# Performance work log

Measured on AMD Instinct MI355X. Metric: run time of the kernel, lower is better.

Reference implementation:

```python
import jax, jax.numpy as jnp
import numpy as np
import math
from jax import lax

HIDDEN = 512
BETA = 1.0
MAX_ITERATIONS = 5
CONV_THRESH = 1e-4
SCALE = BETA / math.sqrt(HIDDEN)


def setup_inputs() -> dict:
    key = jax.random.key(0)
    ks = jax.random.split(key, 9)
    B, S, H = 4, 2048, HIDDEN
    w = 1.0 / math.sqrt(H)  # roughly nn.Linear init scale
    return {
        "x": jax.random.normal(ks[0], (B, S, H), jnp.float32),
        "Wq": jax.random.normal(ks[1], (H, H), jnp.float32) * w,
        "bq": jax.random.normal(ks[2], (H,), jnp.float32) * w,
        "Wk": jax.random.normal(ks[3], (H, H), jnp.float32) * w,
        "bk": jax.random.normal(ks[4], (H,), jnp.float32) * w,
        "Wv": jax.random.normal(ks[5], (H, H), jnp.float32) * w,
        "bv": jax.random.normal(ks[6], (H,), jnp.float32) * w,
        "Wo": jax.random.normal(ks[7], (H, H), jnp.float32) * w,
        "bo": jax.random.normal(ks[8], (H,), jnp.float32) * w,
    }


def _hopfield_update(state, keys):
    # scores: [B, S, S]
    scores = jnp.einsum('bsh,bth->bst', state, keys) * SCALE
    attn = jax.nn.softmax(scores, axis=-1)
    return jnp.einsum('bst,bth->bsh', attn, keys)


def reference(x, Wq, bq, Wk, bk, Wv, bv, Wo, bo):
    query = x @ Wq.T + bq
    keys = x @ Wk.T + bk
    values = x @ Wv.T + bv

    # Iterative Hopfield loop: torch breaks after the update that converges.
    # We run a fixed-length scan, freezing state once converged (same math).
    def step(carry, _):
        state, converged, iters = carry
        new_state = _hopfield_update(state, keys)
        # global Frobenius norms, matching torch.norm over the whole tensor
        delta = jnp.linalg.norm(new_state - state) / (jnp.linalg.norm(state) + 1e-8)
        active = jnp.logical_not(converged)
        state = jnp.where(active, new_state, state)
        iters = iters + active.astype(jnp.int32)
        converged = converged | (active & (delta < CONV_THRESH))
        return (state, converged, iters), None

    init = (query, jnp.array(False), jnp.array(0, jnp.int32))
    (state, converged, iterations), _ = lax.scan(step, init, None, length=MAX_ITERATIONS)

    # Final readout attention against values
    scores = jnp.einsum('bsh,bth->bst', state, keys) * SCALE
    attn = jax.nn.softmax(scores, axis=-1)
    out = jnp.einsum('bst,bth->bsh', attn, values)
    out = out @ Wo.T + bo  # dropout p=0.0 / eval: identity
    return out, iterations, converged
```

## Files before the change

### kernel.cpp

```cpp
#include <hip/hip_runtime.h>
#include <hip/hip_bf16.h>
#include <math.h>

#define HH 512
#define BB 4
#define SS 2048
#define NN (BB*SS)
#define SCALE_F 0.04419417382415922f
#define THRESH 1e-4f
#define CTL_FLOATS 1024

typedef __attribute__((ext_vector_type(8))) short bf16x8;
typedef __attribute__((ext_vector_type(4))) float f32x4;

struct Ctl { float sum_d; float sum_o; int iters; int conv; int cur; int bf[10]; };

__device__ __forceinline__ float b2f(unsigned short u) {
    union { unsigned int i; float f; } c; c.i = ((unsigned int)u) << 16; return c.f;
}
__device__ __forceinline__ unsigned short f2b(float f) {
    unsigned int x = __float_as_uint(f);
    unsigned int r = (x + 0x7FFFu + ((x >> 16) & 1u)) >> 16;
    return (unsigned short)r;
}
__device__ __forceinline__ void splitf(float x, unsigned short& h, unsigned short& l) {
    h = f2b(x);
    l = f2b(x - b2f(h));
}
__device__ __forceinline__ f32x4 MF(bf16x8 a, bf16x8 b, f32x4 c) {
    return __builtin_amdgcn_mfma_f32_16x16x32_bf16(a, b, c, 0, 0, 0);
}

#define FBAR() do { \
    asm volatile("s_waitcnt lgkmcnt(0)" ::: "memory"); \
    __builtin_amdgcn_s_barrier(); \
    asm volatile("" ::: "memory"); \
} while (0)

#define LD4(R, ph, pl) do { \
    const unsigned short* _ph = (ph); const unsigned short* _pl = (pl); \
    R##0 = *(const uint4*)(_ph); R##1 = *(const uint4*)(_ph + 8); \
    R##2 = *(const uint4*)(_pl); R##3 = *(const uint4*)(_pl + 8); \
} while (0)
#define ST4(dh, dl, R) do { \
    unsigned short* _dh = (dh); unsigned short* _dl = (dl); \
    *(uint4*)(_dh) = R##0; *(uint4*)(_dh + 8) = R##1; \
    *(uint4*)(_dl) = R##2; *(uint4*)(_dl + 8) = R##3; \
} while (0)

__global__ __launch_bounds__(256) void detect_dtypes(
        const void* p0, const void* p1, const void* p2, const void* p3, const void* p4,
        const void* p5, const void* p6, const void* p7, const void* p8, Ctl* sc)
{
    const void* ps[9] = {p0,p1,p2,p3,p4,p5,p6,p7,p8};
    const int   ns[9] = {NN*HH, HH*HH, HH, HH*HH, HH, HH*HH, HH, HH*HH, HH};
    const int i = blockIdx.x;
    const unsigned short* u = (const unsigned short*)ps[i];
    const int n = ns[i] < 4096 ? ns[i] : 4096;
    __shared__ int cnt;
    if (threadIdx.x == 0) cnt = 0;
    __syncthreads();
    int c = 0;
    for (int j = threadIdx.x; j < n; j += 256) {
        const int e = (u[j] >> 7) & 0xFF;
        if (e < 32 || e >= 224) ++c;
    }
    if (c) atomicAdd(&cnt, c);
    __syncthreads();
    if (threadIdx.x == 0) sc->bf[i] = (cnt * 16 < n) ? 1 : 0;
}

__global__ __launch_bounds__(64) void init_flags(Ctl* sc) {
    if (threadIdx.x == 0) {
        sc->iters = 0; sc->conv = 0; sc->cur = 0; sc->sum_d = 0.f; sc->sum_o = 0.f;
        int any = 0;
        for (int i = 0; i < 9; ++i) any |= sc->bf[i];
        sc->bf[9] = any;
    }
}

__global__ __launch_bounds__(256) void mfma_gemm(
    const void* __restrict__ Xv, int xIdx,
    const void* __restrict__ Wv, int wIdx,
    const void* __restrict__ Bv, int bIdx,
    float* __restrict__ outF, void* __restrict__ outExt,
    unsigned short* __restrict__ pKH, unsigned short* __restrict__ pKL,
    unsigned short* __restrict__ pKTH, unsigned short* __restrict__ pKTL,
    float* __restrict__ S0w, float* __restrict__ S1w,
    int mode, const Ctl* __restrict__ sc)
{
    __shared__ unsigned short Xh[64][72], Xl[64][72], Wh[64][72], Wl[64][72];
    const int tid = threadIdx.x;
    const int cur = sc->cur;
    const void* Xp = (xIdx == -2) ? (const void*)(cur ? S1w : S0w) : Xv;
    const bool xbf = (xIdx >= 0) && (sc->bf[xIdx] != 0);
    const bool wbf = (sc->bf[wIdx] != 0);
    const bool bbf = (sc->bf[bIdx] != 0);
    const bool obf = (mode == 1) && (sc->bf[9] != 0);
    const bool xs = !xbf, ws = !wbf;

    const int m0 = blockIdx.x * 64, n0 = blockIdx.y * 64;
    const int lane = tid & 63, w = tid >> 6;
    const int mi = w & 1, ni = w >> 1;
    const int quad = lane >> 4, l16 = lane & 15;
    const int srow = tid >> 2, skb = (tid & 3) * 16;

    f32x4 acc[2][2];
    #pragma unroll
    for (int a = 0; a < 2; ++a)
        #pragma unroll
        for (int bq = 0; bq < 2; ++bq) acc[a][bq] = (f32x4){0.f, 0.f, 0.f, 0.f};

    for (int kc = 0; kc < HH; kc += 64) {
        __syncthreads();
        {
            float v[16];
            if (xbf) {
                const unsigned short* p = (const unsigned short*)Xp + (size_t)(m0 + srow)*HH + kc + skb;
                #pragma unroll
                for (int i = 0; i < 4; ++i) {
                    ushort4 t = *(const ushort4*)(p + 4*i);
                    v[4*i]=b2f(t.x); v[4*i+1]=b2f(t.y); v[4*i+2]=b2f(t.z); v[4*i+3]=b2f(t.w);
                }
            } else {
                const float* p = (const float*)Xp + (size_t)(m0 + srow)*HH + kc + skb;
                #pragma unroll
                for (int i = 0; i < 4; ++i) {
                    float4 t = *(const float4*)(p + 4*i);
                    v[4*i]=t.x; v[4*i+1]=t.y; v[4*i+2]=t.z; v[4*i+3]=t.w;
                }
            }
            #pragma unroll
            for (int i = 0; i < 4; ++i) {
                unsigned short h[4], l[4];
                #pragma unroll
                for (int j = 0; j < 4; ++j) splitf(v[4*i+j], h[j], l[j]);
                *(ushort4*)&Xh[srow][skb + 4*i] = make_ushort4(h[0], h[1], h[2], h[3]);
                if (xs) *(ushort4*)&Xl[srow][skb + 4*i] = make_ushort4(l[0], l[1], l[2], l[3]);
            }
        }
        {
            float v[16];
            if (wbf) {
                const unsigned short* p = (const unsigned short*)Wv + (size_t)(n0 + srow)*HH + kc + skb;
                #pragma unroll
                for (int i = 0; i < 4; ++i) {
                    ushort4 t = *(const ushort4*)(p + 4*i);
                    v[4*i]=b2f(t.x); v[4*i+1]=b2f(t.y); v[4*i+2]=b2f(t.z); v[4*i+3]=b2f(t.w);
                }
            } else {
                const float* p = (const float*)Wv + (size_t)(n0 + srow)*HH + kc + skb;
                #pragma unroll
                for (int i = 0; i < 4; ++i) {
                    float4 t = *(const float4*)(p + 4*i);
                    v[4*i]=t.x; v[4*i+1]=t.y; v[4*i+2]=t.z; v[4*i+3]=t.w;
                }
            }
            #pragma unroll
            for (int i = 0; i < 4; ++i) {
                unsigned short h[4], l[4];
                #pragma unroll
                for (int j = 0; j < 4; ++j) splitf(v[4*i+j], h[j], l[j]);
                *(ushort4*)&Wh[srow][skb + 4*i] = make_ushort4(h[0], h[1], h[2], h[3]);
                if (ws) *(ushort4*)&Wl[srow][skb + 4*i] = make_ushort4(l[0], l[1], l[2], l[3]);
            }
        }
        __syncthreads();
        #pragma unroll
        for (int d = 0; d < 2; ++d) {
            const int kl = 32*d + quad*8;
            #pragma unroll
            for (int mt = 0; mt < 2; ++mt) {
                const int xr = 32*mi + 16*mt + l16;
                bf16x8 ahx = *(const bf16x8*)&Xh[xr][kl];
                bf16x8 alx;
                if (xs) alx = *(const bf16x8*)&Xl[xr][kl];
                #pragma unroll
                for (int nt = 0; nt < 2; ++nt) {
                    const int wr = 32*ni + 16*nt + l16;
                    bf16x8 bh = *(const bf16x8*)&Wh[wr][kl];
                    acc[mt][nt] = MF(ahx, bh, acc[mt][nt]);
                    if (xs) acc[mt][nt] = MF(alx, bh, acc[mt][nt]);
                    if (ws) {
                        bf16x8 bl = *(const bf16x8*)&Wl[wr][kl];
                        acc[mt][nt] = MF(ahx, bl, acc[mt][nt]);
                    }
                }
            }
        }
    }
    unsigned short* vtH = nullptr;
    if (mode == 4) { vtH = (unsigned short*)(cur ? S0w : S1w); }
    #pragma unroll
    for (int nt = 0; nt < 2; ++nt) {
        const int col = n0 + 32*ni + 16*nt + l16;
        const float bv = bbf ? b2f(((const unsigned short*)Bv)[col]) : ((const float*)Bv)[col];
        #pragma unroll
        for (int mt = 0; mt < 2; ++mt)
            #pragma unroll
            for (int e = 0; e < 4; ++e) {
                const int row = m0 + 32*mi + 16*mt + quad*4 + e;
                const float vv = acc[mt][nt][e] + bv;
                const size_t idx = (size_t)row*HH + col;
                if (mode == 0) outF[idx] = vv;
                else if (mode == 1) {
                    if (obf) ((unsigned short*)outExt)[idx] = f2b(vv);
                    else     ((float*)outExt)[idx] = vv;
                } else {
                    unsigned short h, l; splitf(vv, h, l);
                    const size_t t = ((size_t)(row >> 11) * HH + col) * SS + (row & 2047);
                    if (mode == 3) {
                        pKH[idx] = h; pKL[idx] = l;
                        pKTH[t] = h;  pKTL[t] = l;
                    } else {
                        vtH[t] = h; vtH[(size_t)NN*HH + t] = l;
                    }
                }
            }
    }
}

template<bool FINAL>
__global__ __launch_bounds__(512, 2) void mfma_attn(
    float* __restrict__ S0w, float* __restrict__ S1w,
    const unsigned short* __restrict__ KH, const unsigned short* __restrict__ KL,
    const unsigned short* __restrict__ KTH, const unsigned short* __restrict__ KTL,
    Ctl* sc)
{
    if constexpr (!FINAL) { if (sc->conv) return; }
    const int cur = sc->cur;
    float* Scur = cur ? S1w : S0w;
    float* Out  = FINAL ? Scur : (cur ? S0w : S1w);
    const unsigned short* VTH = FINAL ? (const unsigned short*)(cur ? S0w : S1w) : KTH;
    const unsigned short* VTL = FINAL ? (VTH + (size_t)NN*HH) : KTL;

    __shared__ __align__(16) unsigned short UB0[18432];
    __shared__ __align__(16) unsigned short UB1[18432];
    __shared__ __align__(16) unsigned short SHl[32*520];
    __shared__ __align__(16) unsigned short Pth[32*72], Ptl[32*72];
    __shared__ __align__(16) float Sld[32*68];
    __shared__ __align__(16) float mld[32], lld[32], ald[32];
    __shared__ float redd[8], redo[8];

    const int tid = threadIdx.x;
    const int lane = tid & 63, w = tid >> 6;
    const int quad = lane >> 4, l16 = lane & 15;
    const int r = w & 1, s = w >> 1;

    const int bid = blockIdx.x;
    const int e8 = bid & 7;
    const int b = e8 >> 1;
    const int q0 = 32 * ((bid >> 3) + 32 * (e8 & 1));

    const size_t bSSHH = (size_t)b * SS * HH;
    const size_t bHHSS = (size_t)b * HH * SS;

    const int key = tid >> 3, hs = (tid & 7) * 16;
    const int rw = tid >> 2, k1 = (tid & 3) * 16;

    const unsigned short* pSH = KH + bSSHH + (size_t)key*HH + hs;
    const unsigned short* pSL = KL + bSSHH + (size_t)key*HH + hs;
    const size_t vbase = bHHSS + (size_t)(128*(rw >> 5) + (rw & 31))*SS + k1;
    const unsigned short* pVH = VTH + vbase;
    const unsigned short* pVL = VTL + vbase;

    uint4 Ra0, Ra1, Ra2, Ra3;
    uint4 Rb0, Rb1, Rb2, Rb3;
    LD4(Ra, pSH, pSL);
    LD4(Rb, pSH + 128, pSL + 128);

    bf16x8 ah[16];
    {
        const float* Qr = Scur + ((size_t)b*SS + q0 + 16*r + l16) * HH + quad*8;
        #pragma unroll
        for (int f = 0; f < 16; ++f) {
            float4 v0 = *(const float4*)(Qr + 32*f);
            float4 v1 = *(const float4*)(Qr + 32*f + 4);
            unsigned short h[8], l[8];
            splitf(v0.x,h[0],l[0]); splitf(v0.y,h[1],l[1]); splitf(v0.z,h[2],l[2]); splitf(v0.w,h[3],l[3]);
            splitf(v1.x,h[4],l[4]); splitf(v1.y,h[5],l[5]); splitf(v1.z,h[6],l[6]); splitf(v1.w,h[7],l[7]);
            bf16x8 af;
            #pragma unroll
            for (int j = 0; j < 8; ++j) af[j] = (short)h[j];
            ah[f] = af;
            if (s == 0) {
                unsigned short* d = &SHl[(16*r + l16)*520 + 32*f + quad*8];
                *(ushort4*)(d)     = make_ushort4(l[0], l[1], l[2], l[3]);
                *(ushort4*)(d + 4) = make_ushort4(l[4], l[5], l[6], l[7]);
            }
        }
        if (tid < 32) { mld[tid] = -INFINITY; lld[tid] = 0.f; }
    }

    f32x4 O[8];
    #pragma unroll
    for (int i = 0; i < 8; ++i) O[i] = (f32x4){0.f, 0.f, 0.f, 0.f};

    const int shlbase = (16*r + l16)*520 + quad*8;

    for (int kt = 0; kt < SS/64; ++kt) {
        const size_t so = (size_t)kt*64*HH;
        const size_t po = (size_t)kt*64;
        f32x4 sA = (f32x4){0.f,0.f,0.f,0.f}, sB = (f32x4){0.f,0.f,0.f,0.f};
        #pragma unroll
        for (int c = 0; c < 4; ++c) {
            unsigned short* ub = (c & 1) ? UB1 : UB0;
            if ((c & 1) == 0) {
                ST4(ub + key*136 + hs, ub + 8704 + key*136 + hs, Ra);
                if (c == 0) LD4(Ra, pSH + so + 2*128, pSL + so + 2*128);
                else        LD4(Ra, pVH + po, pVL + po);
            } else {
                ST4(ub + key*136 + hs, ub + 8704 + key*136 + hs, Rb);
                if (c == 1) LD4(Rb, pSH + so + 3*128, pSL + so + 3*128);
                else        LD4(Rb, pVH + (size_t)32*SS + po, pVL + (size_t)32*SS + po);
            }
            FBAR();
            #pragma unroll
            for (int kf = 0; kf < 4; ++kf) {
                bf16x8 alf = *(const bf16x8*)&SHl[shlbase + c*128 + kf*32];
                const int c0 = kf*32 + quad*8;
                bf16x8 bh = *(const bf16x8*)&ub[(16*s + l16)*136 + c0];
                bf16x8 bl = *(const bf16x8*)&ub[8704 + (16*s + l16)*136 + c0];
                const bf16x8 a = ah[c*4 + kf];
                if (kf & 1) {
                    sB = MF(a, bh, sB); sB = MF(alf, bh, sB); sB = MF(a, bl, sB);
                } else {
                    sA = MF(a, bh, sA); sA = MF(alf, bh, sA); sA = MF(a, bl, sA);
                }
            }
        }
        f32x4 sacc = sA + sB;
        #pragma unroll
        for (int e = 0; e < 4; ++e)
            Sld[(16*r + quad*4 + e)*68 + 16*s + l16] = sacc[e] * SCALE_F;
        FBAR();
        {
            const int row = tid >> 4, sg = tid & 15;
            const float* sr = Sld + row*68 + sg*4;
            float4 x0 = *(const float4*)(sr);
            float mt = fmaxf(fmaxf(x0.x, x0.y), fmaxf(x0.z, x0.w));
            #pragma unroll
            for (int mk = 1; mk < 16; mk <<= 1) mt = fmaxf(mt, __shfl_xor(mt, mk, 16));
            const float mprev = mld[row];
            const float mnew = fmaxf(mprev, mt);
            float p[4];
            p[0]=__expf(x0.x-mnew); p[1]=__expf(x0.y-mnew); p[2]=__expf(x0.z-mnew); p[3]=__expf(x0.w-mnew);
            float ps = p[0]+p[1]+p[2]+p[3];
            #pragma unroll
            for (int mk = 1; mk < 16; mk <<= 1) ps += __shfl_xor(ps, mk, 16);
            const float alpha = __expf(mprev - mnew);
            if (sg == 0) { mld[row] = mnew; lld[row] = lld[row]*alpha + ps; ald[row] = alpha; }
            unsigned short h[4], l[4];
            #pragma unroll
            for (int i = 0; i < 4; ++i) splitf(p[i], h[i], l[i]);
            *(ushort4*)&Pth[row*72 + sg*4] = make_ushort4(h[0],h[1],h[2],h[3]);
            *(ushort4*)&Ptl[row*72 + sg*4] = make_ushort4(l[0],l[1],l[2],l[3]);
        }
        FBAR();
        {
            const float4 av = *(const float4*)&ald[16*r + 4*quad];
            const float a4[4] = {av.x, av.y, av.z, av.w};
            #pragma unroll
            for (int i = 0; i < 8; ++i)
                #pragma unroll
                for (int e = 0; e < 4; ++e) O[i][e] *= a4[e];
        }
        bf16x8 pah[2], pal[2];
        #pragma unroll
        for (int kf = 0; kf < 2; ++kf) {
            pah[kf] = *(const bf16x8*)&Pth[(16*r + l16)*72 + kf*32 + quad*8];
            pal[kf] = *(const bf16x8*)&Ptl[(16*r + l16)*72 + kf*32 + quad*8];
        }
        #pragma unroll
        for (int c = 0; c < 4; ++c) {
            unsigned short* ub = (c & 1) ? UB1 : UB0;
            if ((c & 1) == 0) {
                ST4(ub + rw*72 + k1, ub + 9216 + rw*72 + k1, Ra);
                if (c == 0)             LD4(Ra, pVH + (size_t)64*SS + po, pVL + (size_t)64*SS + po);
                else if (kt+1 < SS/64)  LD4(Ra, pSH + so + (size_t)64*HH,
                                             pSL + so + (size_t)64*HH);
            } else {
                ST4(ub + rw*72 + k1, ub + 9216 + rw*72 + k1, Rb);
                if (c == 1)             LD4(Rb, pVH + (size_t)96*SS + po, pVL + (size_t)96*SS + po);
                else if (kt+1 < SS/64)  LD4(Rb, pSH + so + (size_t)64*HH + 128,
                                             pSL + so + (size_t)64*HH + 128);
            }
            FBAR();
            #pragma unroll
            for (int nt = 0; nt < 2; ++nt) {
                const int rb = (32*s + 16*nt + l16)*72;
                #pragma unroll
                for (int kf = 0; kf < 2; ++kf) {
                    bf16x8 bh = *(const bf16x8*)&ub[rb + kf*32 + quad*8];
                    bf16x8 bl = *(const bf16x8*)&ub[9216 + rb + kf*32 + quad*8];
                    O[c*2+nt] = MF(pah[kf], bh, O[c*2+nt]);
                    O[c*2+nt] = MF(pal[kf], bh, O[c*2+nt]);
                    O[c*2+nt] = MF(pah[kf], bl, O[c*2+nt]);
                }
            }
        }
    }
    const float4 lv = *(const float4*)&lld[16*r + 4*quad];
    const float inv[4] = {1.f/lv.x, 1.f/lv.y, 1.f/lv.z, 1.f/lv.w};
    float pd = 0.f, po2 = 0.f;
    #pragma unroll
    for (int c = 0; c < 4; ++c)
        #pragma unroll
        for (int nt = 0; nt < 2; ++nt)
            #pragma unroll
            for (int e = 0; e < 4; ++e) {
                const int row = q0 + 16*r + quad*4 + e;
                const int col = 128*s + 32*c + 16*nt + l16;
                const float nv = O[c*2+nt][e] * inv[e];
                const size_t idx = (size_t)b*SS*HH + (size_t)row*HH + col;
                if constexpr (!FINAL) {
                    const float old = Scur[idx];
                    const float d = nv - old;
                    pd += d*d; po2 += old*old;
                }
                Out[idx] = nv;
            }
    if constexpr (!FINAL) {
        #pragma unroll
        for (int mk = 1; mk < 64; mk <<= 1) {
            pd  += __shfl_xor(pd, mk, 64);
            po2 += __shfl_xor(po2, mk, 64);
        }
        if (lane == 0) { redd[w] = pd; redo[w] = po2; }
        __syncthreads();
        if (tid == 0) {
            float td = 0.f, to = 0.f;
            #pragma unroll
            for (int i = 0; i < 8; ++i) { td += redd[i]; to += redo[i]; }
            atomicAdd(&sc->sum_d, td);
            atomicAdd(&sc->sum_o, to);
        }
    }
}

__global__ __launch_bounds__(64) void flag_update(Ctl* sc) {
    if (threadIdx.x != 0) return;
    if (sc->conv) return;
    sc->cur ^= 1;
    sc->iters += 1;
    const float delta = sqrtf(sc->sum_d) / (sqrtf(sc->sum_o) + 1e-8f);
    if (delta < THRESH) sc->conv = 1;
    sc->sum_d = 0.f; sc->sum_o = 0.f;
}

__global__ __launch_bounds__(64) void write_scalars(const Ctl* sc, void* outv) {
    if (threadIdx.x != 0) return;
    if (sc->bf[9]) {
        unsigned short* o = (unsigned short*)outv;
        o[(size_t)NN*HH]     = f2b((float)sc->iters);
        o[(size_t)NN*HH + 1] = f2b(sc->conv ? 1.0f : 0.0f);
    } else {
        float* o = (float*)outv;
        o[(size_t)NN*HH]     = (float)sc->iters;
        o[(size_t)NN*HH + 1] = sc->conv ? 1.0f : 0.0f;
    }
}

extern "C" void kernel_launch(void* const* d_in, const int* in_sizes, int n_in,
                              void* d_out, int out_size, void* d_ws, size_t ws_size,
                              hipStream_t stream)
{
    const void* x  = d_in[0];
    const void* Wq = d_in[1];
    const void* bq = d_in[2];
    const void* Wk = d_in[3];
    const void* bk = d_in[4];
    const void* Wv = d_in[5];
    const void* bv = d_in[6];
    const void* Wo = d_in[7];
    const void* bo = d_in[8];

    Ctl* sc = (Ctl*)d_ws;
    float* S0 = (float*)d_ws + CTL_FLOATS;
    float* S1 = S0 + (size_t)NN*HH;
    unsigned short* KH  = (unsigned short*)(S1 + (size_t)NN*HH);
    unsigned short* KL  = KH  + (size_t)NN*HH;
    unsigned short* KTH = KL  + (size_t)NN*HH;
    unsigned short* KTL = KTH + (size_t)NN*HH;

    const dim3 ggrid(NN/64, HH/64);
    const int  agrid = 256;

    detect_dtypes<<<9, 256, 0, stream>>>(x, Wq, bq, Wk, bk, Wv, bv, Wo, bo, sc);
    init_flags<<<1, 64, 0, stream>>>(sc);

    mfma_gemm<<<ggrid, 256, 0, stream>>>(x, 0, Wq, 1, bq, 2, S0, nullptr,
                                         nullptr, nullptr, nullptr, nullptr, S0, S1, 0, sc);
    mfma_gemm<<<ggrid, 256, 0, stream>>>(x, 0, Wk, 3, bk, 4, nullptr, nullptr,
                                         KH, KL, KTH, KTL, S0, S1, 3, sc);

    for (int it = 0; it < 5; ++it) {
        mfma_attn<false><<<agrid, 512, 0, stream>>>(S0, S1, KH, KL, KTH, KTL, sc);
        flag_update<<<1, 64, 0, stream>>>(sc);
    }

    mfma_gemm<<<ggrid, 256, 0, stream>>>(x, 0, Wv, 5, bv, 6, nullptr, nullptr,
                                         nullptr, nullptr, nullptr, nullptr, S0, S1, 4, sc);
    mfma_attn<true><<<agrid, 512, 0, stream>>>(S0, S1, KH, KL, KTH, KTL, sc);
    mfma_gemm<<<ggrid, 256, 0, stream>>>(nullptr, -2, Wo, 7, bo, 8, nullptr, d_out,
                                         nullptr, nullptr, nullptr, nullptr, S0, S1, 1, sc);
    if (out_size >= (int)((size_t)NN*HH + 2))
        write_scalars<<<1, 64, 0, stream>>>(sc, d_out);
}
```

Measured before the change: 1.277 ms.

## Stage K/V tiles in two larger chunks and keep query low parts in registers

The attention kernel now stages each 64-key tile in two half-width chunks of 256 hidden columns instead of four 128-column chunks. This halves the barriers per phase, and each thread loads twice as many bytes per prefetch. The low-precision query split is held in registers (al[16]) instead of shared memory, which removes an LDS read per MFMA group. The cost is much higher register pressure (eight uint4 staging registers plus sixteen more bf16x8) and larger LDS buffers, which may reduce occupancy under launch_bounds(512,2) or cause spills.

```diff
diff --git a/kernel.cpp b/kernel.cpp
--- a/kernel.cpp
+++ b/kernel.cpp
@@ -37,15 +37,19 @@
     asm volatile("" ::: "memory"); \
 } while (0)
 
-#define LD4(R, ph, pl) do { \
+#define LD8(R, ph, pl) do { \
     const unsigned short* _ph = (ph); const unsigned short* _pl = (pl); \
-    R##0 = *(const uint4*)(_ph); R##1 = *(const uint4*)(_ph + 8); \
-    R##2 = *(const uint4*)(_pl); R##3 = *(const uint4*)(_pl + 8); \
+    R##0 = *(const uint4*)(_ph);      R##1 = *(const uint4*)(_ph + 8); \
+    R##2 = *(const uint4*)(_ph + 16); R##3 = *(const uint4*)(_ph + 24); \
+    R##4 = *(const uint4*)(_pl);      R##5 = *(const uint4*)(_pl + 8); \
+    R##6 = *(const uint4*)(_pl + 16); R##7 = *(const uint4*)(_pl + 24); \
 } while (0)
-#define ST4(dh, dl, R) do { \
+#define ST8(dh, dl, R) do { \
     unsigned short* _dh = (dh); unsigned short* _dl = (dl); \
-    *(uint4*)(_dh) = R##0; *(uint4*)(_dh + 8) = R##1; \
-    *(uint4*)(_dl) = R##2; *(uint4*)(_dl + 8) = R##3; \
+    *(uint4*)(_dh)      = R##0; *(uint4*)(_dh + 8)  = R##1; \
+    *(uint4*)(_dh + 16) = R##2; *(uint4*)(_dh + 24) = R##3; \
+    *(uint4*)(_dl)      = R##4; *(uint4*)(_dl + 8)  = R##5; \
+    *(uint4*)(_dl + 16) = R##6; *(uint4*)(_dl + 24) = R##7; \
 } while (0)
 
 __global__ __launch_bounds__(256) void detect_dtypes(
@@ -234,9 +238,8 @@
     const unsigned short* VTH = FINAL ? (const unsigned short*)(cur ? S0w : S1w) : KTH;
     const unsigned short* VTL = FINAL ? (VTH + (size_t)NN*HH) : KTL;
 
-    __shared__ __align__(16) unsigned short UB0[18432];
-    __shared__ __align__(16) unsigned short UB1[18432];
-    __shared__ __align__(16) unsigned short SHl[32*520];
+    __shared__ __align__(16) unsigned short UB0[34816];
+    __shared__ __align__(16) unsigned short UB1[34816];
     __shared__ __align__(16) unsigned short Pth[32*72], Ptl[32*72];
     __shared__ __align__(16) float Sld[32*68];
     __shared__ __align__(16) float mld[32], lld[32], ald[32];
@@ -255,21 +258,19 @@
     const size_t bSSHH = (size_t)b * SS * HH;
     const size_t bHHSS = (size_t)b * HH * SS;
 
-    const int key = tid >> 3, hs = (tid & 7) * 16;
-    const int rw = tid >> 2, k1 = (tid & 3) * 16;
+    const int key = tid >> 3, hs = (tid & 7) * 32;
+    const int rw2 = tid >> 1, kc2 = (tid & 1) * 32;
 
     const unsigned short* pSH = KH + bSSHH + (size_t)key*HH + hs;
     const unsigned short* pSL = KL + bSSHH + (size_t)key*HH + hs;
-    const size_t vbase = bHHSS + (size_t)(128*(rw >> 5) + (rw & 31))*SS + k1;
-    const unsigned short* pVH = VTH + vbase;
-    const unsigned short* pVL = VTL + vbase;
-
-    uint4 Ra0, Ra1, Ra2, Ra3;
-    uint4 Rb0, Rb1, Rb2, Rb3;
-    LD4(Ra, pSH, pSL);
-    LD4(Rb, pSH + 128, pSL + 128);
-
-    bf16x8 ah[16];
+    const int vhid0 = 128*(rw2 >> 6) + 32*((rw2 >> 5) & 1) + (rw2 & 31);
+    const unsigned short* pVH = VTH + bHHSS + (size_t)vhid0*SS + kc2;
+    const unsigned short* pVL = VTL + bHHSS + (size_t)vhid0*SS + kc2;
+
+    uint4 Ra0, Ra1, Ra2, Ra3, Ra4, Ra5, Ra6, Ra7;
+    LD8(Ra, pSH, pSL);
+
+    bf16x8 ah[16], al[16];
     {
         const float* Qr = Scur + ((size_t)b*SS + q0 + 16*r + l16) * HH + quad*8;
         #pragma unroll
@@ -279,15 +280,10 @@
             unsigned short h[8], l[8];
             splitf(v0.x,h[0],l[0]); splitf(v0.y,h[1],l[1]); splitf(v0.z,h[2],l[2]); splitf(v0.w,h[3],l[3]);
             splitf(v1.x,h[4],l[4]); splitf(v1.y,h[5],l[5]); splitf(v1.z,h[6],l[6]); splitf(v1.w,h[7],l[7]);
-            bf16x8 af;
-            #pragma unroll
-            for (int j = 0; j < 8; ++j) af[j] = (short)h[j];
-            ah[f] = af;
-            if (s == 0) {
-                unsigned short* d = &SHl[(16*r + l16)*520 + 32*f + quad*8];
-                *(ushort4*)(d)     = make_ushort4(l[0], l[1], l[2], l[3]);
-                *(ushort4*)(d + 4) = make_ushort4(l[4], l[5], l[6], l[7]);
-            }
+            bf16x8 af, bf;
+            #pragma unroll
+            for (int j = 0; j < 8; ++j) { af[j] = (short)h[j]; bf[j] = (short)l[j]; }
+            ah[f] = af; al[f] = bf;
         }
         if (tid < 32) { mld[tid] = -INFINITY; lld[tid] = 0.f; }
     }
@@ -295,37 +291,29 @@
     f32x4 O[8];
     #pragma unroll
     for (int i = 0; i < 8; ++i) O[i] = (f32x4){0.f, 0.f, 0.f, 0.f};
-
-    const int shlbase = (16*r + l16)*520 + quad*8;
 
     for (int kt = 0; kt < SS/64; ++kt) {
         const size_t so = (size_t)kt*64*HH;
         const size_t po = (size_t)kt*64;
         f32x4 sA = (f32x4){0.f,0.f,0.f,0.f}, sB = (f32x4){0.f,0.f,0.f,0.f};
         #pragma unroll
-        for (int c = 0; c < 4; ++c) {
-            unsigned short* ub = (c & 1) ? UB1 : UB0;
-            if ((c & 1) == 0) {
-                ST4(ub + key*136 + hs, ub + 8704 + key*136 + hs, Ra);
-                if (c == 0) LD4(Ra, pSH + so + 2*128, pSL + so + 2*128);
-                else        LD4(Ra, pVH + po, pVL + po);
-            } else {
-                ST4(ub + key*136 + hs, ub + 8704 + key*136 + hs, Rb);
-                if (c == 1) LD4(Rb, pSH + so + 3*128, pSL + so + 3*128);
-                else        LD4(Rb, pVH + (size_t)32*SS + po, pVL + (size_t)32*SS + po);
-            }
+        for (int p = 0; p < 2; ++p) {
+            unsigned short* ub = p ? UB1 : UB0;
+            ST8(ub + key*260 + hs, ub + 16640 + key*260 + hs, Ra);
+            if (p == 0) LD8(Ra, pSH + so + 256, pSL + so + 256);
+            else        LD8(Ra, pVH + po, pVL + po);
             FBAR();
             #pragma unroll
-            for (int kf = 0; kf < 4; ++kf) {
-                bf16x8 alf = *(const bf16x8*)&SHl[shlbase + c*128 + kf*32];
+            for (int kf = 0; kf < 8; ++kf) {
                 const int c0 = kf*32 + quad*8;
-                bf16x8 bh = *(const bf16x8*)&ub[(16*s + l16)*136 + c0];
-                bf16x8 bl = *(const bf16x8*)&ub[8704 + (16*s + l16)*136 + c0];
-                const bf16x8 a = ah[c*4 + kf];
+                bf16x8 bh = *(const bf16x8*)&ub[(16*s + l16)*260 + c0];
+                bf16x8 bl = *(const bf16x8*)&ub[16640 + (16*s + l16)*260 + c0];
+                const bf16x8 a  = ah[8*p + kf];
+                const bf16x8 af = al[8*p + kf];
                 if (kf & 1) {
-                    sB = MF(a, bh, sB); sB = MF(alf, bh, sB); sB = MF(a, bl, sB);
+                    sB = MF(a, bh, sB); sB = MF(af, bh, sB); sB = MF(a, bl, sB);
                 } else {
-                    sA = MF(a, bh, sA); sA = MF(alf, bh, sA); sA = MF(a, bl, sA);
+                    sA = MF(a, bh, sA); sA = MF(af, bh, sA); sA = MF(a, bl, sA);
                 }
             }
         }
@@ -372,32 +360,27 @@
             pal[kf] = *(const bf16x8*)&Ptl[(16*r + l16)*72 + kf*32 + quad*8];
         }
         #pragma unroll
-        for (int c = 0; c < 4; ++c) {
-            unsigned short* ub = (c & 1) ? UB1 : UB0;
-            if ((c & 1) == 0) {
-                ST4(ub + rw*72 + k1, ub + 9216 + rw*72 + k1, Ra);
-                if (c == 0)             LD4(Ra, pVH + (size_t)64*SS + po, pVL + (size_t)64*SS + po);
-                else if (kt+1 < SS/64)  LD4(Ra, pSH + so + (size_t)64*HH,
-                                             pSL + so + (size_t)64*HH);
-            } else {
-                ST4(ub + rw*72 + k1, ub + 9216 + rw*72 + k1, Rb);
-                if (c == 1)             LD4(Rb, pVH + (size_t)96*SS + po, pVL + (size_t)96*SS + po);
-                else if (kt+1 < SS/64)  LD4(Rb, pSH + so + (size_t)64*HH + 128,
-                                             pSL + so + (size_t)64*HH + 128);
-            }
+        for (int p = 0; p < 2; ++p) {
+            unsigned short* ub = p ? UB1 : UB0;
+            ST8(ub + rw2*68 + kc2, ub + 17408 + rw2*68 + kc2, Ra);
+            if (p == 0)             LD8(Ra, pVH + (size_t)64*SS + po, pVL + (size_t)64*SS + po);
+            else if (kt+1 < SS/64)  LD8(Ra, pSH + so + (size_t)64*HH, pSL + so + (size_t)64*HH);
             FBAR();
             #pragma unroll
-            for (int nt = 0; nt < 2; ++nt) {
-                const int rb = (32*s + 16*nt + l16)*72;
-                #pragma unroll
-                for (int kf = 0; kf < 2; ++kf) {
-                    bf16x8 bh = *(const bf16x8*)&ub[rb + kf*32 + quad*8];
-                    bf16x8 bl = *(const bf16x8*)&ub[9216 + rb + kf*32 + quad*8];
-                    O[c*2+nt] = MF(pah[kf], bh, O[c*2+nt]);
-                    O[c*2+nt] = MF(pal[kf], bh, O[c*2+nt]);
-                    O[c*2+nt] = MF(pah[kf], bl, O[c*2+nt]);
-                }
-            }
+            for (int cp = 0; cp < 2; ++cp)
+                #pragma unroll
+                for (int nt = 0; nt < 2; ++nt) {
+                    const int rb = (64*s + 32*cp + 16*nt + l16)*68;
+                    const int oi = (2*p + cp)*2 + nt;
+                    #pragma unroll
+                    for (int kf = 0; kf < 2; ++kf) {
+                        bf16x8 bh = *(const bf16x8*)&ub[rb + kf*32 + quad*8];
+                        bf16x8 bl = *(const bf16x8*)&ub[17408 + rb + kf*32 + quad*8];
+                        O[oi] = MF(pah[kf], bh, O[oi]);
+                        O[oi] = MF(pal[kf], bh, O[oi]);
+                        O[oi] = MF(pah[kf], bl, O[oi]);
+                    }
+                }
         }
     }
     const float4 lv = *(const float4*)&lld[16*r + 4*quad];
```

New measurement: 4.407 ms. 3.45x slower.

## Stage K/V tiles via direct global-to-LDS loads with XOR swizzle

Applied to the files above, without the earlier changes.

Replaces the register-staged global loads plus LDS stores in the attention kernel with global_load_lds direct-to-LDS transfers, double-buffered across UB0/UB1. Padded LDS layouts are replaced by unpadded tiles with an XOR swizzle to avoid bank conflicts, which shrinks the shared buffers. This removes VGPR pressure and explicit ds_write instructions, at the cost of waiting on vmcnt(0) at every barrier, so prefetch depth is limited to one stage.

```diff
diff --git a/kernel.cpp b/kernel.cpp
--- a/kernel.cpp
+++ b/kernel.cpp
@@ -31,21 +31,21 @@
     return __builtin_amdgcn_mfma_f32_16x16x32_bf16(a, b, c, 0, 0, 0);
 }
 
+typedef __attribute__((address_space(1))) const unsigned int gu32;
+typedef __attribute__((address_space(3))) unsigned int lu32;
+__device__ __forceinline__ void gl_lds16(const unsigned short* g, unsigned short* l) {
+    __builtin_amdgcn_global_load_lds((gu32*)g, (lu32*)l, 16, 0, 0);
+}
+
+#define SBAR() do { \
+    asm volatile("s_waitcnt vmcnt(0) lgkmcnt(0)" ::: "memory"); \
+    __builtin_amdgcn_s_barrier(); \
+    asm volatile("" ::: "memory"); \
+} while (0)
 #define FBAR() do { \
     asm volatile("s_waitcnt lgkmcnt(0)" ::: "memory"); \
     __builtin_amdgcn_s_barrier(); \
     asm volatile("" ::: "memory"); \
-} while (0)
-
-#define LD4(R, ph, pl) do { \
-    const unsigned short* _ph = (ph); const unsigned short* _pl = (pl); \
-    R##0 = *(const uint4*)(_ph); R##1 = *(const uint4*)(_ph + 8); \
-    R##2 = *(const uint4*)(_pl); R##3 = *(const uint4*)(_pl + 8); \
-} while (0)
-#define ST4(dh, dl, R) do { \
-    unsigned short* _dh = (dh); unsigned short* _dl = (dl); \
-    *(uint4*)(_dh) = R##0; *(uint4*)(_dh + 8) = R##1; \
-    *(uint4*)(_dl) = R##2; *(uint4*)(_dl + 8) = R##3; \
 } while (0)
 
 __global__ __launch_bounds__(256) void detect_dtypes(
@@ -234,8 +234,8 @@
     const unsigned short* VTH = FINAL ? (const unsigned short*)(cur ? S0w : S1w) : KTH;
     const unsigned short* VTL = FINAL ? (VTH + (size_t)NN*HH) : KTL;
 
-    __shared__ __align__(16) unsigned short UB0[18432];
-    __shared__ __align__(16) unsigned short UB1[18432];
+    __shared__ __align__(16) unsigned short UB0[16384];
+    __shared__ __align__(16) unsigned short UB1[16384];
     __shared__ __align__(16) unsigned short SHl[32*520];
     __shared__ __align__(16) unsigned short Pth[32*72], Ptl[32*72];
     __shared__ __align__(16) float Sld[32*68];
@@ -255,19 +255,32 @@
     const size_t bSSHH = (size_t)b * SS * HH;
     const size_t bHHSS = (size_t)b * HH * SS;
 
-    const int key = tid >> 3, hs = (tid & 7) * 16;
-    const int rw = tid >> 2, k1 = (tid & 3) * 16;
-
-    const unsigned short* pSH = KH + bSSHH + (size_t)key*HH + hs;
-    const unsigned short* pSL = KL + bSSHH + (size_t)key*HH + hs;
-    const size_t vbase = bHHSS + (size_t)(128*(rw >> 5) + (rw & 31))*SS + k1;
-    const unsigned short* pVH = VTH + vbase;
-    const unsigned short* pVL = VTL + vbase;
-
-    uint4 Ra0, Ra1, Ra2, Ra3;
-    uint4 Rb0, Rb1, Rb2, Rb3;
-    LD4(Ra, pSH, pSL);
-    LD4(Rb, pSH + 128, pSL + 128);
+    const int keyS = 4*w + quad;
+    const int swS  = ((lane & 15) ^ (keyS & 7)) * 8;
+    const int r3   = lane >> 3;
+    const int swP  = ((lane & 7) ^ (r3 & 7)) * 8;
+    const int rowP = 8*w + r3;
+    const int hidP0 = 128*(rowP >> 5) + (rowP & 31);
+    const int hidP1 = 128*(2 + (rowP >> 5)) + (rowP & 31);
+
+    auto stageS = [&](int c, int kt, unsigned short* ub) {
+        const size_t g0 = bSSHH + (size_t)(kt*64 + keyS)*HH + c*128 + swS;
+        const size_t g1 = bSSHH + (size_t)(kt*64 + keyS + 32)*HH + c*128 + swS;
+        gl_lds16(KH + g0, ub +                 w*64*8);
+        gl_lds16(KH + g1, ub +        4096 +   w*64*8);
+        gl_lds16(KL + g0, ub + 8192 +          w*64*8);
+        gl_lds16(KL + g1, ub + 8192 + 4096 +   w*64*8);
+    };
+    auto stageP = [&](int c, int kt, unsigned short* ub) {
+        const size_t g0 = bHHSS + (size_t)(hidP0 + 32*c)*SS + (size_t)kt*64 + swP;
+        const size_t g1 = bHHSS + (size_t)(hidP1 + 32*c)*SS + (size_t)kt*64 + swP;
+        gl_lds16(VTH + g0, ub +                 w*64*8);
+        gl_lds16(VTH + g1, ub +        4096 +   w*64*8);
+        gl_lds16(VTL + g0, ub + 8192 +          w*64*8);
+        gl_lds16(VTL + g1, ub + 8192 + 4096 +   w*64*8);
+    };
+
+    stageS(0, 0, UB0);
 
     bf16x8 ah[16];
     {
@@ -299,28 +312,19 @@
     const int shlbase = (16*r + l16)*520 + quad*8;
 
     for (int kt = 0; kt < SS/64; ++kt) {
-        const size_t so = (size_t)kt*64*HH;
-        const size_t po = (size_t)kt*64;
         f32x4 sA = (f32x4){0.f,0.f,0.f,0.f}, sB = (f32x4){0.f,0.f,0.f,0.f};
         #pragma unroll
         for (int c = 0; c < 4; ++c) {
             unsigned short* ub = (c & 1) ? UB1 : UB0;
-            if ((c & 1) == 0) {
-                ST4(ub + key*136 + hs, ub + 8704 + key*136 + hs, Ra);
-                if (c == 0) LD4(Ra, pSH + so + 2*128, pSL + so + 2*128);
-                else        LD4(Ra, pVH + po, pVL + po);
-            } else {
-                ST4(ub + key*136 + hs, ub + 8704 + key*136 + hs, Rb);
-                if (c == 1) LD4(Rb, pSH + so + 3*128, pSL + so + 3*128);
-                else        LD4(Rb, pVH + (size_t)32*SS + po, pVL + (size_t)32*SS + po);
-            }
-            FBAR();
+            SBAR();
+            if (c < 3) stageS(c+1, kt, (c & 1) ? UB0 : UB1);
+            else       stageP(0, kt, UB0);
             #pragma unroll
             for (int kf = 0; kf < 4; ++kf) {
                 bf16x8 alf = *(const bf16x8*)&SHl[shlbase + c*128 + kf*32];
-                const int c0 = kf*32 + quad*8;
-                bf16x8 bh = *(const bf16x8*)&ub[(16*s + l16)*136 + c0];
-                bf16x8 bl = *(const bf16x8*)&ub[8704 + (16*s + l16)*136 + c0];
+                const int cc = ((4*kf + quad) ^ (l16 & 7)) * 8;
+                bf16x8 bh = *(const bf16x8*)&ub[(16*s + l16)*128 + cc];
+                bf16x8 bl = *(const bf16x8*)&ub[8192 + (16*s + l16)*128 + cc];
                 const bf16x8 a = ah[c*4 + kf];
                 if (kf & 1) {
                     sB = MF(a, bh, sB); sB = MF(alf, bh, sB); sB = MF(a, bl, sB);
@@ -374,25 +378,17 @@
         #pragma unroll
         for (int c = 0; c < 4; ++c) {
             unsigned short* ub = (c & 1) ? UB1 : UB0;
-            if ((c & 1) == 0) {
-                ST4(ub + rw*72 + k1, ub + 9216 + rw*72 + k1, Ra);
-                if (c == 0)             LD4(Ra, pVH + (size_t)64*SS + po, pVL + (size_t)64*SS + po);
-                else if (kt+1 < SS/64)  LD4(Ra, pSH + so + (size_t)64*HH,
-                                             pSL + so + (size_t)64*HH);
-            } else {
-                ST4(ub + rw*72 + k1, ub + 9216 + rw*72 + k1, Rb);
-                if (c == 1)             LD4(Rb, pVH + (size_t)96*SS + po, pVL + (size_t)96*SS + po);
-                else if (kt+1 < SS/64)  LD4(Rb, pSH + so + (size_t)64*HH + 128,
-                                             pSL + so + (size_t)64*HH + 128);
-            }
-            FBAR();
+            SBAR();
+            if (c < 3)              stageP(c+1, kt, (c & 1) ? UB0 : UB1);
+            else if (kt+1 < SS/64)  stageS(0, kt+1, UB0);
             #pragma unroll
             for (int nt = 0; nt < 2; ++nt) {
-                const int rb = (32*s + 16*nt + l16)*72;
+                const int rb = (32*s + 16*nt + l16)*64;
                 #pragma unroll
                 for (int kf = 0; kf < 2; ++kf) {
-                    bf16x8 bh = *(const bf16x8*)&ub[rb + kf*32 + quad*8];
-                    bf16x8 bl = *(const bf16x8*)&ub[9216 + rb + kf*32 + quad*8];
+                    const int cc = ((4*kf + quad) ^ (l16 & 7)) * 8;
+                    bf16x8 bh = *(const bf16x8*)&ub[rb + cc];
+                    bf16x8 bl = *(const bf16x8*)&ub[8192 + rb + cc];
                     O[c*2+nt] = MF(pah[kf], bh, O[c*2+nt]);
                     O[c*2+nt] = MF(pal[kf], bh, O[c*2+nt]);
                     O[c*2+nt] = MF(pah[kf], bl, O[c*2+nt]);
```

Measured after the change: 1.577 ms. 1.24x slower.
